# Performance work log

Measured on AMD Instinct MI355X. Metric: run time of the kernel, lower is better.

## Reference

```python
import jax, jax.numpy as jnp
import numpy as np

D_MODEL = 2048
N_HEADS = 16
HEAD_DIM = 128
WINDOW = 256
B, T = 2, 2048
SCALE = float(np.sqrt(HEAD_DIM))


def setup_inputs() -> dict:
    key = jax.random.key(0)
    ks = jax.random.split(key, 5)
    init = 0.02
    x = jax.random.normal(ks[0], (B, T, D_MODEL), dtype=jnp.float32)
    Wq = jax.random.normal(ks[1], (D_MODEL, D_MODEL), dtype=jnp.float32) * init
    Wk = jax.random.normal(ks[2], (D_MODEL, D_MODEL), dtype=jnp.float32) * init
    Wv = jax.random.normal(ks[3], (D_MODEL, D_MODEL), dtype=jnp.float32) * init
    Wo = jax.random.normal(ks[4], (D_MODEL, D_MODEL), dtype=jnp.float32) * init
    return {"x": x, "Wq": Wq, "Wk": Wk, "Wv": Wv, "Wo": Wo}


def _allowed_mask():
    # [H, T, T] bool: global (even) heads -> causal; local (odd) heads -> causal band of WINDOW
    idx = jnp.arange(T)
    causal = idx[None, :] <= idx[:, None]                      # [T, T]
    band = idx[None, :] >= (idx[:, None] - WINDOW + 1)         # [T, T]
    is_global = (jnp.arange(N_HEADS) % 2) == 0                 # [H]
    return causal[None] & (is_global[:, None, None] | band[None])


def reference(x, Wq, Wk, Wv, Wo):
    # projections (nn.Linear: y = x @ W.T), reshape to [B, H, T, D]
    def proj(W):
        return (x @ W.T).reshape(B, T, N_HEADS, HEAD_DIM).transpose(0, 2, 1, 3)

    q, k, v = proj(Wq), proj(Wk), proj(Wv)
    scores = jnp.einsum("bhtd,bhsd->bhts", q, k) / SCALE       # [B, H, T, T]
    allowed = _allowed_mask()                                  # [H, T, T]
    neg_inf = jnp.asarray(-jnp.inf, dtype=scores.dtype)
    scores = jnp.where(allowed[None], scores, neg_inf)
    attn = jax.nn.softmax(scores, axis=-1)
    out = jnp.einsum("bhts,bhsd->bhtd", attn, v)               # [B, H, T, D]
    concat = out.transpose(0, 2, 1, 3).reshape(B, T, N_HEADS * HEAD_DIM)
    return concat @ Wo.T
```

## Files before the change

kernel.cpp:

```cpp
#include <hip/hip_runtime.h>

typedef __attribute__((ext_vector_type(4))) float f32x4;
typedef __attribute__((ext_vector_type(8))) short bf16x8;
typedef __attribute__((ext_vector_type(4))) unsigned short u16x4;
typedef unsigned short u16;

#define MFMA16(a, b, c) __builtin_amdgcn_mfma_f32_16x16x32_bf16((a), (b), (c), 0, 0, 0)

#define T_SEQ 2048
#define DMODEL 2048
#define NHEADS 16
#define HDIM 128
#define WINDOW 256
#define MROWS 4096
#define SC 0.08838834764831845f

__device__ __forceinline__ u16 f2bf(float f) {
  union { float f; unsigned u; } v; v.f = f;
  return (u16)((v.u + 0x7FFFu + ((v.u >> 16) & 1u)) >> 16);
}
__device__ __forceinline__ float bf2f(u16 u) {
  union { unsigned u; float f; } v; v.u = ((unsigned)u) << 16;
  return v.f;
}
__device__ __forceinline__ void gl_lds16(const u16* g, u16* l) {
  __builtin_amdgcn_global_load_lds((const __attribute__((address_space(1))) void*)(g),
                                   (__attribute__((address_space(3))) void*)(l), 16, 0, 0);
}

#define BAR __builtin_amdgcn_s_barrier()
#define FEN asm volatile("" ::: "memory")
#define VMC3 asm volatile("s_waitcnt vmcnt(3)" ::: "memory")
#define VMC2 asm volatile("s_waitcnt vmcnt(2)" ::: "memory")
#define VMC0 asm volatile("s_waitcnt vmcnt(0)" ::: "memory")

__global__ __launch_bounds__(256) void convert_all(const float* __restrict__ x,
                                                   const float* __restrict__ wq,
                                                   const float* __restrict__ wk,
                                                   const float* __restrict__ wv,
                                                   const float* __restrict__ wo,
                                                   u16* __restrict__ dst) {
  const size_t NX = (size_t)MROWS * DMODEL;
  const size_t NW = (size_t)DMODEL * DMODEL;
  const size_t chunks = (NX + 4 * NW) / 8;
  for (size_t ci = (size_t)blockIdx.x * 256 + threadIdx.x; ci < chunks;
       ci += (size_t)gridDim.x * 256) {
    const size_t off = ci * 8;
    const float* src;
    size_t so;
    if (off < NX) { src = x; so = off; }
    else {
      size_t rem = off - NX;
      if (rem < NW) { src = wq; so = rem; }
      else if (rem < 2 * NW) { src = wk; so = rem - NW; }
      else if (rem < 3 * NW) { src = wv; so = rem - 2 * NW; }
      else { src = wo; so = rem - 3 * NW; }
    }
    f32x4 a = *(const f32x4*)&src[so];
    f32x4 b = *(const f32x4*)&src[so + 4];
    bf16x8 o;
#pragma unroll
    for (int j = 0; j < 4; ++j) { o[j] = (short)f2bf(a[j]); o[j + 4] = (short)f2bf(b[j]); }
    *(bf16x8*)&dst[off] = o;
  }
}

__global__ __launch_bounds__(512, 2) void gemm_qkv(const u16* __restrict__ A,
                                                   const u16* __restrict__ W,
                                                   u16* __restrict__ qb,
                                                   u16* __restrict__ kb,
                                                   u16* __restrict__ vb) {
  __shared__ u16 lds[57344];
  const int tid = threadIdx.x, w = tid >> 6, lane = tid & 63;
  const int wm = w >> 2, wn = w & 3;
  const int fr = lane & 15, g = lane >> 4, g4 = g * 4;

  const int xcd = blockIdx.x & 7, bi = blockIdx.x >> 3;
  const int mt = bi >> 2, nt = xcd * 4 + (bi & 3);
  const int m0 = mt * 256, n0 = nt * 192;

  const int xs0 = (g ^ (fr & 7)) * 8;
  const int xs1 = xs0 ^ 32;
  const int aRow = wm * 128 + fr;
  const int bRow = wn * 48 + fr;

  const int sr = tid >> 3;
  const int scc = ((tid & 7) ^ (sr & 7)) * 8;
  const u16* pA0  = A + (size_t)(m0 + sr) * DMODEL + scc;
  const u16* pA1  = A + (size_t)(m0 + 64 + sr) * DMODEL + scc;
  const u16* pB0  = W + (size_t)(n0 + sr) * DMODEL + scc;
  const u16* pB0b = W + (size_t)(n0 + 64 + sr) * DMODEL + scc;
  const u16* pB1  = W + (size_t)(n0 + 128 + sr) * DMODEL + scc;

#define SAH(h, t, c)                                                                   \
  { gl_lds16(pA0 + (size_t)(h) * 128 * DMODEL + (t) * 64,                              \
             &lds[(c) * 16384 + (h) * 8192 + w * 512]);                                \
    gl_lds16(pA1 + (size_t)(h) * 128 * DMODEL + (t) * 64,                              \
             &lds[(c) * 16384 + (h) * 8192 + 4096 + w * 512]); }
#define SBH0(t, c)                                                                     \
  { gl_lds16(pB0 + (size_t)(t) * 64, &lds[32768 + (c) * 12288 + w * 512]);             \
    gl_lds16(pB0b + (size_t)(t) * 64, &lds[32768 + (c) * 12288 + 4096 + w * 512]); }
#define SBH1(t, c)                                                                     \
  { gl_lds16(pB1 + (size_t)(t) * 64, &lds[32768 + (c) * 12288 + 8192 + w * 512]); }

#define RD_AL(c)                                                                       \
  { _Pragma("unroll") for (int m_ = 0; m_ < 4; ++m_) {                                 \
      af[m_][0] = *(const bf16x8*)&lds[(c) * 16384 + (aRow + m_ * 16) * 64 + xs0];     \
      af[m_][1] = *(const bf16x8*)&lds[(c) * 16384 + (aRow + m_ * 16) * 64 + xs1]; } }
#define RD_AH(c)                                                                       \
  { _Pragma("unroll") for (int m_ = 0; m_ < 4; ++m_) {                                 \
      af[m_][0] = *(const bf16x8*)&lds[(c) * 16384 + (aRow + 64 + m_ * 16) * 64 + xs0];\
      af[m_][1] = *(const bf16x8*)&lds[(c) * 16384 + (aRow + 64 + m_ * 16) * 64 + xs1]; } }
#define RD_B(c)                                                                        \
  { _Pragma("unroll") for (int n_ = 0; n_ < 3; ++n_) {                                 \
      bfr[n_][0] = *(const bf16x8*)&lds[32768 + (c) * 12288 + (bRow + n_ * 16) * 64 + xs0]; \
      bfr[n_][1] = *(const bf16x8*)&lds[32768 + (c) * 12288 + (bRow + n_ * 16) * 64 + xs1]; } }

#define MMQ(MB)                                                                        \
  { __builtin_amdgcn_s_setprio(1);                                                    \
    _Pragma("unroll") for (int kc_ = 0; kc_ < 2; ++kc_)                                \
      _Pragma("unroll") for (int m_ = 0; m_ < 4; ++m_)                                 \
        _Pragma("unroll") for (int n_ = 0; n_ < 3; ++n_)                               \
          acc[(MB) + m_][n_] = MFMA16(af[m_][kc_], bfr[n_][kc_], acc[(MB) + m_][n_]);  \
    __builtin_amdgcn_s_setprio(0); }

  bf16x8 af[4][2], bfr[3][2];
  f32x4 acc[8][3];
#pragma unroll
  for (int i = 0; i < 8; ++i)
#pragma unroll
    for (int j = 0; j < 3; ++j) acc[i][j] = (f32x4){0.f, 0.f, 0.f, 0.f};

  SAH(0, 0, 0); SAH(1, 0, 0);
  SBH0(0, 0); SBH1(0, 0);
  SBH0(1, 1); SBH1(1, 1);
  VMC3; BAR;

#pragma unroll 1
  for (int i = 0; i < 15; ++i) {
    const int t0 = 2 * i;
    RD_AL(0); RD_B(0); SAH(0, t0 + 1, 1); SAH(1, t0 + 1, 1);
    FEN; BAR; MMQ(0); FEN; BAR;
    RD_AH(0); SBH0(t0 + 2, 0); SBH1(t0 + 2, 0);
    VMC3; BAR; MMQ(4); FEN; BAR;
    RD_AL(1); RD_B(1); SAH(0, t0 + 2, 0); SAH(1, t0 + 2, 0);
    FEN; BAR; MMQ(0); FEN; BAR;
    RD_AH(1); SBH0(t0 + 3, 1); SBH1(t0 + 3, 1);
    VMC3; BAR; MMQ(4); FEN; BAR;
  }
  RD_AL(0); RD_B(0); SAH(0, 31, 1); SAH(1, 31, 1);
  FEN; BAR; MMQ(0); FEN; BAR;
  RD_AH(0);
  VMC0; BAR; MMQ(4); FEN; BAR;
  RD_AL(1); RD_B(1);
  FEN; BAR; MMQ(0); FEN; BAR;
  RD_AH(1);
  FEN; BAR; MMQ(4);

#pragma unroll
  for (int mi = 0; mi < 8; ++mi)
#pragma unroll
    for (int ni = 0; ni < 3; ++ni) {
      const int row0 = m0 + wm * 128 + mi * 16 + g4;
      const int cg = n0 + wn * 48 + ni * 16 + fr;
      const int bb = row0 >> 11, tl = row0 & 2047;
      if (cg < DMODEL) {
#pragma unroll
        for (int r = 0; r < 4; ++r)
          qb[(size_t)(row0 + r) * DMODEL + cg] = f2bf(acc[mi][ni][r] * SC);
      } else if (cg < 2 * DMODEL) {
        const int cc = cg - DMODEL;
        const int hh = cc >> 7, d = cc & 127;
        const size_t kbase = (size_t)(bb * NHEADS + hh) * T_SEQ * HDIM;
#pragma unroll
        for (int r = 0; r < 4; ++r)
          kb[kbase + (size_t)(tl + r) * HDIM + d] = f2bf(acc[mi][ni][r]);
      } else {
        const int cc = cg - 2 * DMODEL;
        const int hh = cc >> 7, d = cc & 127;
        u16x4 w4;
#pragma unroll
        for (int r = 0; r < 4; ++r) w4[r] = f2bf(acc[mi][ni][r]);
        *(u16x4*)&vb[(size_t)(bb * NHEADS + hh) * T_SEQ * HDIM + (size_t)(tl >> 6) * 8192 +
                     d * 64 + (tl & 63)] = w4;
      }
    }
#undef SAH
#undef SBH0
#undef SBH1
#undef RD_AL
#undef RD_AH
#undef RD_B
#undef MMQ
}

__global__ __launch_bounds__(512, 2) void gemm_out(const u16* __restrict__ A,
                                                   const u16* __restrict__ W0,
                                                   float* __restrict__ outf) {
  __shared__ u16 lds2[49152];
  const int tid = threadIdx.x, w = tid >> 6, lane = tid & 63;
  const int wm = w >> 2, wn = w & 3;
  const int fr = lane & 15, g = lane >> 4, g4 = g * 4;

  const int xcd = blockIdx.x & 7, bi = blockIdx.x >> 3;
  const int mt = bi >> 1, nt = xcd * 2 + (bi & 1);
  const int m0 = mt * 256, n0 = nt * 128;

  const int xs0 = (g ^ (fr & 7)) * 8;
  const int xs1 = xs0 ^ 32;
  const int aRow = wm * 128 + fr;
  const int bRow = wn * 32 + fr;

  const int sr = tid >> 3;
  const int scc = ((tid & 7) ^ (sr & 7)) * 8;
  const u16* pA0  = A + (size_t)(m0 + sr) * DMODEL + scc;
  const u16* pA1  = A + (size_t)(m0 + 64 + sr) * DMODEL + scc;
  const u16* pB0  = W0 + (size_t)(n0 + sr) * DMODEL + scc;
  const u16* pB0b = W0 + (size_t)(n0 + 64 + sr) * DMODEL + scc;

#define S2A(h, t, c)                                                                   \
  { gl_lds16(pA0 + (size_t)(h) * 128 * DMODEL + (t) * 64,                              \
             &lds2[(c) * 16384 + (h) * 8192 + w * 512]);                               \
    gl_lds16(pA1 + (size_t)(h) * 128 * DMODEL + (t) * 64,                              \
             &lds2[(c) * 16384 + (h) * 8192 + 4096 + w * 512]); }
#define S2B(t, c)                                                                      \
  { gl_lds16(pB0 + (size_t)(t) * 64, &lds2[32768 + (c) * 8192 + w * 512]);             \
    gl_lds16(pB0b + (size_t)(t) * 64, &lds2[32768 + (c) * 8192 + 4096 + w * 512]); }

#define R2AL(c)                                                                        \
  { _Pragma("unroll") for (int m_ = 0; m_ < 4; ++m_) {                                 \
      af[m_][0] = *(const bf16x8*)&lds2[(c) * 16384 + (aRow + m_ * 16) * 64 + xs0];    \
      af[m_][1] = *(const bf16x8*)&lds2[(c) * 16384 + (aRow + m_ * 16) * 64 + xs1]; } }
#define R2AH(c)                                                                        \
  { _Pragma("unroll") for (int m_ = 0; m_ < 4; ++m_) {                                 \
      af[m_][0] = *(const bf16x8*)&lds2[(c) * 16384 + (aRow + 64 + m_ * 16) * 64 + xs0]; \
      af[m_][1] = *(const bf16x8*)&lds2[(c) * 16384 + (aRow + 64 + m_ * 16) * 64 + xs1]; } }
#define R2B(c)                                                                         \
  { _Pragma("unroll") for (int n_ = 0; n_ < 2; ++n_) {                                 \
      bfr[n_][0] = *(const bf16x8*)&lds2[32768 + (c) * 8192 + (bRow + n_ * 16) * 64 + xs0]; \
      bfr[n_][1] = *(const bf16x8*)&lds2[32768 + (c) * 8192 + (bRow + n_ * 16) * 64 + xs1]; } }

#define M2(MB)                                                                         \
  { __builtin_amdgcn_s_setprio(1);                                                    \
    _Pragma("unroll") for (int kc_ = 0; kc_ < 2; ++kc_)                                \
      _Pragma("unroll") for (int m_ = 0; m_ < 4; ++m_)                                 \
        _Pragma("unroll") for (int n_ = 0; n_ < 2; ++n_)                               \
          acc[(MB) + m_][n_] = MFMA16(af[m_][kc_], bfr[n_][kc_], acc[(MB) + m_][n_]);  \
    __builtin_amdgcn_s_setprio(0); }

  bf16x8 af[4][2], bfr[2][2];
  f32x4 acc[8][2];
#pragma unroll
  for (int i = 0; i < 8; ++i)
#pragma unroll
    for (int j = 0; j < 2; ++j) acc[i][j] = (f32x4){0.f, 0.f, 0.f, 0.f};

  S2A(0, 0, 0); S2A(1, 0, 0);
  S2B(0, 0);
  S2B(1, 1);
  VMC2; BAR;

#pragma unroll 1
  for (int i = 0; i < 15; ++i) {
    const int t0 = 2 * i;
    R2AL(0); R2B(0); S2A(0, t0 + 1, 1); S2A(1, t0 + 1, 1);
    FEN; BAR; M2(0); FEN; BAR;
    R2AH(0); S2B(t0 + 2, 0);
    VMC2; BAR; M2(4); FEN; BAR;
    R2AL(1); R2B(1); S2A(0, t0 + 2, 0); S2A(1, t0 + 2, 0);
    FEN; BAR; M2(0); FEN; BAR;
    R2AH(1); S2B(t0 + 3, 1);
    VMC2; BAR; M2(4); FEN; BAR;
  }
  R2AL(0); R2B(0); S2A(0, 31, 1); S2A(1, 31, 1);
  FEN; BAR; M2(0); FEN; BAR;
  R2AH(0);
  VMC0; BAR; M2(4); FEN; BAR;
  R2AL(1); R2B(1);
  FEN; BAR; M2(0); FEN; BAR;
  R2AH(1);
  FEN; BAR; M2(4);

#pragma unroll
  for (int mi = 0; mi < 8; ++mi)
#pragma unroll
    for (int ni = 0; ni < 2; ++ni) {
      const int row0 = m0 + wm * 128 + mi * 16 + g4;
      const int c = n0 + wn * 32 + ni * 16 + fr;
#pragma unroll
      for (int r = 0; r < 4; ++r)
        outf[(size_t)(row0 + r) * DMODEL + c] = acc[mi][ni][r];
    }
#undef S2A
#undef S2B
#undef R2AL
#undef R2AH
#undef R2B
#undef M2
}

#define QB 128
#define KVB 64

__global__ __launch_bounds__(512, 4) void attn_kernel(const u16* __restrict__ qb,
                                                      const u16* __restrict__ kb,
                                                      const u16* __restrict__ vb,
                                                      u16* __restrict__ op,
                                                      u16* __restrict__ pO,
                                                      float* __restrict__ pm,
                                                      float* __restrict__ pl) {
  __shared__ u16 lds[40960];

  const int bx = blockIdx.x, h = blockIdx.y, b = blockIdx.z;
  const bool isglobal = (h & 1) == 0;
  int qt, klo, khi, part = 0;
  bool partial = false;
  if (isglobal) {
    if (bx < 16) {
      qt = 15 - (bx >> 1);
      part = bx & 1;
      partial = true;
      if (part == 0) { klo = 0; khi = 15; } else { klo = 16; khi = 2 * qt + 1; }
    } else {
      qt = 23 - bx;
      klo = 0; khi = 2 * qt + 1;
    }
  } else {
    if (bx >= 16) return;
    qt = 15 - bx;
    const int lo_ = qt * QB - (WINDOW - 1);
    klo = lo_ > 0 ? (lo_ >> 6) : 0;
    khi = 2 * qt + 1;
  }

  const int tid = threadIdx.x, wave = tid >> 6, lane = tid & 63;
  const int fr = lane & 15, g = lane >> 4, g4 = g * 4;
  const int xk = fr & 7;
  const int q0 = qt * QB;
  const int bh = b * NHEADS + h;
  const size_t basek = (size_t)bh * T_SEQ * HDIM;
  const size_t baseo = (size_t)b * T_SEQ * DMODEL + (size_t)h * HDIM;

  bf16x8 qf[4];
  {
    const int qrow = q0 + wave * 16 + fr;
#pragma unroll
    for (int ds = 0; ds < 4; ++ds)
      qf[ds] = *(const bf16x8*)&qb[(size_t)b * T_SEQ * DMODEL + (size_t)qrow * DMODEL +
                                   (size_t)h * HDIM + ds * 32 + g * 8];
  }

  float mrun = -1e30f, lrun = 0.f;
  f32x4 o[8];
#pragma unroll
  for (int dt = 0; dt < 8; ++dt) o[dt] = (f32x4){0.f, 0.f, 0.f, 0.f};

  const int j0 = wave * 2, j1 = wave * 2 + 1;
  const int gi0 = j0 * 64 + lane, gi1 = j1 * 64 + lane;
  const int kr0 = gi0 >> 4, kc0 = (gi0 & 15) ^ (kr0 & 7);
  const int kr1 = gi1 >> 4, kc1 = (gi1 & 15) ^ (kr1 & 7);
  const u16* pK0 = kb + basek + (size_t)kr0 * HDIM + kc0 * 8;
  const u16* pK1 = kb + basek + (size_t)kr1 * HDIM + kc1 * 8;
  const int d0 = gi0 >> 3, vs0 = (gi0 & 7) ^ (d0 & 7);
  const int d1 = gi1 >> 3, vs1 = (gi1 & 7) ^ (d1 & 7);
  const u16* pV0 = vb + basek + (size_t)d0 * 64 + vs0 * 8;
  const u16* pV1 = vb + basek + (size_t)d1 * 64 + vs1 * 8;

#define STAGE(KT, c)                                                                   \
  { gl_lds16(pK0 + (size_t)(KT) * 8192, &lds[(c) * 8192 + j0 * 512]);                  \
    gl_lds16(pK1 + (size_t)(KT) * 8192, &lds[(c) * 8192 + j1 * 512]);                  \
    gl_lds16(pV0 + (size_t)(KT) * 8192, &lds[16384 + (c) * 8192 + j0 * 512]);          \
    gl_lds16(pV1 + (size_t)(KT) * 8192, &lds[16384 + (c) * 8192 + j1 * 512]); }

  u16* Pw = &lds[32768 + wave * 1024];
  const int qg = q0 + wave * 16 + fr;

  STAGE(klo, klo & 1);
  VMC0; BAR;

  for (int kt = klo; kt <= khi; ++kt) {
    const int c = kt & 1;
    const bool more = kt < khi;
    if (more) STAGE(kt + 1, c ^ 1);
    const u16* Kc = &lds[c * 8192];
    const u16* Vc = &lds[16384 + c * 8192];

    f32x4 s[4];
    __builtin_amdgcn_s_setprio(1);
#pragma unroll
    for (int kk = 0; kk < 4; ++kk) {
      f32x4 a = (f32x4){0.f, 0.f, 0.f, 0.f};
#pragma unroll
      for (int ds = 0; ds < 4; ++ds) {
        const int r = kk * 16 + fr;
        bf16x8 kf = *(const bf16x8*)&Kc[r * 128 + (((ds * 4 + g) ^ xk) << 3)];
        a = MFMA16(kf, qf[ds], a);
      }
      s[kk] = a;
    }
    __builtin_amdgcn_s_setprio(0);

    float sv[16];
    float pmax = -1e30f;
#pragma unroll
    for (int kk = 0; kk < 4; ++kk)
#pragma unroll
      for (int reg = 0; reg < 4; ++reg) {
        const int cg = kt * KVB + kk * 16 + g4 + reg;
        const bool allowed = (cg <= qg) && (isglobal || cg >= qg - (WINDOW - 1));
        const float v = allowed ? s[kk][reg] : -1e30f;
        sv[kk * 4 + reg] = v;
        pmax = fmaxf(pmax, v);
      }
    pmax = fmaxf(pmax, __shfl_xor(pmax, 16, 64));
    pmax = fmaxf(pmax, __shfl_xor(pmax, 32, 64));
    const bool resc = !__all(pmax - mrun <= 8.0f);
    float fac = 1.f;
    if (resc) {
      const float nm = fmaxf(mrun, pmax);
      fac = __expf(mrun - nm);
      mrun = nm;
    }
    float rs = 0.f;
    u16 pb[16];
#pragma unroll
    for (int i = 0; i < 16; ++i) {
      const float p = (sv[i] > -5e29f) ? __expf(sv[i] - mrun) : 0.f;
      rs += p;
      pb[i] = f2bf(p);
    }
    rs += __shfl_xor(rs, 16, 64);
    rs += __shfl_xor(rs, 32, 64);
    lrun = lrun * fac + rs;

#pragma unroll
    for (int kk = 0; kk < 4; ++kk) {
      u16x4 wv;
      wv[0] = pb[kk * 4]; wv[1] = pb[kk * 4 + 1]; wv[2] = pb[kk * 4 + 2]; wv[3] = pb[kk * 4 + 3];
      *(u16x4*)&Pw[fr * 64 + (((2 * kk + (g >> 1)) ^ xk) << 3) + (g & 1) * 4] = wv;
    }

    if (resc) {
      float ff[4];
#pragma unroll
      for (int r = 0; r < 4; ++r) ff[r] = __shfl(fac, g4 + r, 64);
#pragma unroll
      for (int dt = 0; dt < 8; ++dt)
#pragma unroll
        for (int r = 0; r < 4; ++r) o[dt][r] *= ff[r];
    }

    bf16x8 pf0 = *(const bf16x8*)&Pw[fr * 64 + ((g ^ xk) << 3)];
    bf16x8 pf1 = *(const bf16x8*)&Pw[fr * 64 + (((4 + g) ^ xk) << 3)];
    __builtin_amdgcn_s_setprio(1);
#pragma unroll
    for (int dt = 0; dt < 8; ++dt) {
      const int d = dt * 16 + fr;
      bf16x8 vf0 = *(const bf16x8*)&Vc[d * 64 + ((g ^ xk) << 3)];
      bf16x8 vf1 = *(const bf16x8*)&Vc[d * 64 + (((4 + g) ^ xk) << 3)];
      o[dt] = MFMA16(pf0, vf0, o[dt]);
      o[dt] = MFMA16(pf1, vf1, o[dt]);
    }
    __builtin_amdgcn_s_setprio(0);

    FEN;
    VMC0;
    BAR;
  }

  if (!partial) {
    const float inv = 1.0f / lrun;
    float iv[4];
#pragma unroll
    for (int r = 0; r < 4; ++r) iv[r] = __shfl(inv, g4 + r, 64);
#pragma unroll
    for (int r = 0; r < 4; ++r) {
      const int qrow = q0 + wave * 16 + g4 + r;
#pragma unroll
      for (int dt = 0; dt < 8; ++dt)
        op[baseo + (size_t)qrow * DMODEL + dt * 16 + fr] = f2bf(o[dt][r] * iv[r]);
    }
  } else {
    const int sidx = (((b * 8 + (h >> 1)) * 8 + (qt - 8)) << 1) + part;
    const size_t sb = (size_t)sidx * QB;
#pragma unroll
    for (int r = 0; r < 4; ++r) {
      const size_t row = sb + wave * 16 + g4 + r;
#pragma unroll
      for (int dt = 0; dt < 8; ++dt)
        pO[row * HDIM + dt * 16 + fr] = f2bf(o[dt][r]);
    }
    if (lane < 16) {
      pm[sb + wave * 16 + lane] = mrun;
      pl[sb + wave * 16 + lane] = lrun;
    }
  }
#undef STAGE
}

__global__ __launch_bounds__(256) void merge_kernel(const u16* __restrict__ pO,
                                                    const float* __restrict__ pm,
                                                    const float* __restrict__ pl,
                                                    u16* __restrict__ op) {
  const int x = blockIdx.x;
  const int qt8 = x & 7, eh = (x >> 3) & 7, b = x >> 6;
  const int h = eh * 2, qt = 8 + qt8;
  const int s0 = x * 2, s1 = s0 + 1;

  for (int i = 0; i < 8; ++i) {
    const int vidx = threadIdx.x + i * 256;
    const int row = vidx >> 4, d8 = (vidx & 15) * 8;
    const float m0 = pm[s0 * QB + row], m1 = pm[s1 * QB + row];
    const float l0 = pl[s0 * QB + row], l1 = pl[s1 * QB + row];
    const float m = fmaxf(m0, m1);
    const float w0 = __expf(m0 - m), w1 = __expf(m1 - m);
    const float inv = 1.0f / (l0 * w0 + l1 * w1);
    bf16x8 a = *(const bf16x8*)&pO[((size_t)s0 * QB + row) * HDIM + d8];
    bf16x8 c = *(const bf16x8*)&pO[((size_t)s1 * QB + row) * HDIM + d8];
    bf16x8 r;
#pragma unroll
    for (int j = 0; j < 8; ++j)
      r[j] = (short)f2bf((bf2f((u16)a[j]) * w0 + bf2f((u16)c[j]) * w1) * inv);
    *(bf16x8*)&op[((size_t)(b * T_SEQ + qt * QB + row)) * DMODEL + h * HDIM + d8] = r;
  }
}

extern "C" void kernel_launch(void* const* d_in, const int* in_sizes, int n_in,
                              void* d_out, int out_size, void* d_ws, size_t ws_size,
                              hipStream_t stream) {
  (void)in_sizes; (void)n_in; (void)out_size; (void)ws_size;
  const float* x  = (const float*)d_in[0];
  const float* Wq = (const float*)d_in[1];
  const float* Wk = (const float*)d_in[2];
  const float* Wv = (const float*)d_in[3];
  const float* Wo = (const float*)d_in[4];

  const size_t NX = (size_t)MROWS * DMODEL;
  const size_t NW = (size_t)DMODEL * DMODEL;
  u16* ws  = (u16*)d_ws;
  u16* xb  = ws;
  u16* wqb = ws + NX;
  u16* wkb = wqb + NW;
  u16* wvb = wkb + NW;
  u16* wob = wvb + NW;
  u16* qbb = wob + NW;
  u16* kbb = qbb + NX;
  u16* vbb = kbb + NX;

  u16*   pO = wqb;
  float* pm = (float*)(wqb + (size_t)256 * QB * HDIM);
  float* pl = pm + 256 * QB;

  convert_all<<<2048, 256, 0, stream>>>(x, Wq, Wk, Wv, Wo, ws);

  gemm_qkv<<<512, 512, 0, stream>>>(xb, wqb, qbb, kbb, vbb);

  attn_kernel<<<dim3(24, NHEADS, 2), 512, 0, stream>>>(qbb, kbb, vbb, xb, pO, pm, pl);

  merge_kernel<<<128, 256, 0, stream>>>(pO, pm, pl, xb);

  gemm_out<<<256, 512, 0, stream>>>(xb, wob, (float*)d_out);
}
```

Baseline: 246.7 us.

## Process two 16-row query tiles per wave in attention with 4 waves per block

The attention kernel now runs 4 waves (256 threads) per block, and each wave handles 32 query rows as two 16-row sub-tiles. Each K fragment read from LDS feeds two QK MFMAs and each V fragment feeds two PV MFMAs, halving LDS reads per MFMA. Each wave also issues twice as many global-to-LDS staging loads. Register pressure roughly doubles for accumulators and Q fragments, and there are fewer waves per block to hide latency.

```diff
diff --git a/kernel.cpp b/kernel.cpp
--- a/kernel.cpp
+++ b/kernel.cpp
@@ -302,7 +302,7 @@
 #define QB 128
 #define KVB 64
 
-__global__ __launch_bounds__(512, 4) void attn_kernel(const u16* __restrict__ qb,
+__global__ __launch_bounds__(256, 2) void attn_kernel(const u16* __restrict__ qb,
                                                       const u16* __restrict__ kb,
                                                       const u16* __restrict__ vb,
                                                       u16* __restrict__ op,
@@ -341,39 +341,47 @@
   const size_t basek = (size_t)bh * T_SEQ * HDIM;
   const size_t baseo = (size_t)b * T_SEQ * DMODEL + (size_t)h * HDIM;
 
-  bf16x8 qf[4];
+  bf16x8 qf0[4], qf1[4];
   {
-    const int qrow = q0 + wave * 16 + fr;
-#pragma unroll
-    for (int ds = 0; ds < 4; ++ds)
-      qf[ds] = *(const bf16x8*)&qb[(size_t)b * T_SEQ * DMODEL + (size_t)qrow * DMODEL +
-                                   (size_t)h * HDIM + ds * 32 + g * 8];
-  }
-
-  float mrun = -1e30f, lrun = 0.f;
-  f32x4 o[8];
-#pragma unroll
-  for (int dt = 0; dt < 8; ++dt) o[dt] = (f32x4){0.f, 0.f, 0.f, 0.f};
-
-  const int j0 = wave * 2, j1 = wave * 2 + 1;
-  const int gi0 = j0 * 64 + lane, gi1 = j1 * 64 + lane;
-  const int kr0 = gi0 >> 4, kc0 = (gi0 & 15) ^ (kr0 & 7);
-  const int kr1 = gi1 >> 4, kc1 = (gi1 & 15) ^ (kr1 & 7);
-  const u16* pK0 = kb + basek + (size_t)kr0 * HDIM + kc0 * 8;
-  const u16* pK1 = kb + basek + (size_t)kr1 * HDIM + kc1 * 8;
-  const int d0 = gi0 >> 3, vs0 = (gi0 & 7) ^ (d0 & 7);
-  const int d1 = gi1 >> 3, vs1 = (gi1 & 7) ^ (d1 & 7);
-  const u16* pV0 = vb + basek + (size_t)d0 * 64 + vs0 * 8;
-  const u16* pV1 = vb + basek + (size_t)d1 * 64 + vs1 * 8;
+    const int qr0 = q0 + wave * 32 + fr;
+#pragma unroll
+    for (int ds = 0; ds < 4; ++ds) {
+      qf0[ds] = *(const bf16x8*)&qb[(size_t)b * T_SEQ * DMODEL + (size_t)qr0 * DMODEL +
+                                    (size_t)h * HDIM + ds * 32 + g * 8];
+      qf1[ds] = *(const bf16x8*)&qb[(size_t)b * T_SEQ * DMODEL + (size_t)(qr0 + 16) * DMODEL +
+                                    (size_t)h * HDIM + ds * 32 + g * 8];
+    }
+  }
+
+  float mr0 = -1e30f, lr0 = 0.f, mr1 = -1e30f, lr1 = 0.f;
+  f32x4 o0[8], o1[8];
+#pragma unroll
+  for (int dt = 0; dt < 8; ++dt) {
+    o0[dt] = (f32x4){0.f, 0.f, 0.f, 0.f};
+    o1[dt] = (f32x4){0.f, 0.f, 0.f, 0.f};
+  }
+
+  const u16* pK[4];
+  const u16* pV[4];
+#pragma unroll
+  for (int j = 0; j < 4; ++j) {
+    const int gi = (wave * 4 + j) * 64 + lane;
+    const int kr = gi >> 4, kc = (gi & 15) ^ (kr & 7);
+    pK[j] = kb + basek + (size_t)kr * HDIM + kc * 8;
+    const int d = gi >> 3, vs = (gi & 7) ^ (d & 7);
+    pV[j] = vb + basek + (size_t)d * 64 + vs * 8;
+  }
 
 #define STAGE(KT, c)                                                                   \
-  { gl_lds16(pK0 + (size_t)(KT) * 8192, &lds[(c) * 8192 + j0 * 512]);                  \
-    gl_lds16(pK1 + (size_t)(KT) * 8192, &lds[(c) * 8192 + j1 * 512]);                  \
-    gl_lds16(pV0 + (size_t)(KT) * 8192, &lds[16384 + (c) * 8192 + j0 * 512]);          \
-    gl_lds16(pV1 + (size_t)(KT) * 8192, &lds[16384 + (c) * 8192 + j1 * 512]); }
-
-  u16* Pw = &lds[32768 + wave * 1024];
-  const int qg = q0 + wave * 16 + fr;
+  { _Pragma("unroll") for (int j = 0; j < 4; ++j) {                                    \
+      gl_lds16(pK[j] + (size_t)(KT) * 8192, &lds[(c) * 8192 + (wave * 4 + j) * 512]);  \
+      gl_lds16(pV[j] + (size_t)(KT) * 8192,                                            \
+               &lds[16384 + (c) * 8192 + (wave * 4 + j) * 512]); } }
+
+  u16* Pw0 = &lds[32768 + (wave * 2 + 0) * 1024];
+  u16* Pw1 = &lds[32768 + (wave * 2 + 1) * 1024];
+  const int qg0 = q0 + wave * 32 + fr;
+  const int qg1 = qg0 + 16;
 
   STAGE(klo, klo & 1);
   VMC0; BAR;
@@ -385,81 +393,87 @@
     const u16* Kc = &lds[c * 8192];
     const u16* Vc = &lds[16384 + c * 8192];
 
-    f32x4 s[4];
+    f32x4 s0[4], s1[4];
     __builtin_amdgcn_s_setprio(1);
 #pragma unroll
     for (int kk = 0; kk < 4; ++kk) {
-      f32x4 a = (f32x4){0.f, 0.f, 0.f, 0.f};
+      f32x4 a0 = (f32x4){0.f, 0.f, 0.f, 0.f};
+      f32x4 a1 = (f32x4){0.f, 0.f, 0.f, 0.f};
 #pragma unroll
       for (int ds = 0; ds < 4; ++ds) {
         const int r = kk * 16 + fr;
         bf16x8 kf = *(const bf16x8*)&Kc[r * 128 + (((ds * 4 + g) ^ xk) << 3)];
-        a = MFMA16(kf, qf[ds], a);
+        a0 = MFMA16(kf, qf0[ds], a0);
+        a1 = MFMA16(kf, qf1[ds], a1);
       }
-      s[kk] = a;
+      s0[kk] = a0;
+      s1[kk] = a1;
     }
     __builtin_amdgcn_s_setprio(0);
 
-    float sv[16];
-    float pmax = -1e30f;
-#pragma unroll
-    for (int kk = 0; kk < 4; ++kk)
-#pragma unroll
-      for (int reg = 0; reg < 4; ++reg) {
-        const int cg = kt * KVB + kk * 16 + g4 + reg;
-        const bool allowed = (cg <= qg) && (isglobal || cg >= qg - (WINDOW - 1));
-        const float v = allowed ? s[kk][reg] : -1e30f;
-        sv[kk * 4 + reg] = v;
-        pmax = fmaxf(pmax, v);
-      }
-    pmax = fmaxf(pmax, __shfl_xor(pmax, 16, 64));
-    pmax = fmaxf(pmax, __shfl_xor(pmax, 32, 64));
-    const bool resc = !__all(pmax - mrun <= 8.0f);
-    float fac = 1.f;
-    if (resc) {
-      const float nm = fmaxf(mrun, pmax);
-      fac = __expf(mrun - nm);
-      mrun = nm;
-    }
-    float rs = 0.f;
-    u16 pb[16];
-#pragma unroll
-    for (int i = 0; i < 16; ++i) {
-      const float p = (sv[i] > -5e29f) ? __expf(sv[i] - mrun) : 0.f;
-      rs += p;
-      pb[i] = f2bf(p);
-    }
-    rs += __shfl_xor(rs, 16, 64);
-    rs += __shfl_xor(rs, 32, 64);
-    lrun = lrun * fac + rs;
-
-#pragma unroll
-    for (int kk = 0; kk < 4; ++kk) {
-      u16x4 wv;
-      wv[0] = pb[kk * 4]; wv[1] = pb[kk * 4 + 1]; wv[2] = pb[kk * 4 + 2]; wv[3] = pb[kk * 4 + 3];
-      *(u16x4*)&Pw[fr * 64 + (((2 * kk + (g >> 1)) ^ xk) << 3) + (g & 1) * 4] = wv;
-    }
-
-    if (resc) {
-      float ff[4];
-#pragma unroll
-      for (int r = 0; r < 4; ++r) ff[r] = __shfl(fac, g4 + r, 64);
-#pragma unroll
-      for (int dt = 0; dt < 8; ++dt)
-#pragma unroll
-        for (int r = 0; r < 4; ++r) o[dt][r] *= ff[r];
-    }
-
-    bf16x8 pf0 = *(const bf16x8*)&Pw[fr * 64 + ((g ^ xk) << 3)];
-    bf16x8 pf1 = *(const bf16x8*)&Pw[fr * 64 + (((4 + g) ^ xk) << 3)];
+#define SOFTMAX(SARR, MR, LR, PW, OA, QG)                                              \
+    {                                                                                  \
+      float sv[16];                                                                    \
+      float pmax = -1e30f;                                                             \
+      _Pragma("unroll") for (int kk = 0; kk < 4; ++kk)                                 \
+        _Pragma("unroll") for (int reg = 0; reg < 4; ++reg) {                          \
+          const int cg = kt * KVB + kk * 16 + g4 + reg;                                \
+          const bool allowed = (cg <= (QG)) && (isglobal || cg >= (QG) - (WINDOW - 1));\
+          const float v = allowed ? SARR[kk][reg] : -1e30f;                            \
+          sv[kk * 4 + reg] = v;                                                        \
+          pmax = fmaxf(pmax, v);                                                       \
+        }                                                                              \
+      pmax = fmaxf(pmax, __shfl_xor(pmax, 16, 64));                                    \
+      pmax = fmaxf(pmax, __shfl_xor(pmax, 32, 64));                                    \
+      const bool resc = !__all(pmax - MR <= 8.0f);                                     \
+      float fac = 1.f;                                                                 \
+      if (resc) {                                                                      \
+        const float nm = fmaxf(MR, pmax);                                              \
+        fac = __expf(MR - nm);                                                         \
+        MR = nm;                                                                       \
+      }                                                                                \
+      float rs = 0.f;                                                                  \
+      u16 pb[16];                                                                      \
+      _Pragma("unroll") for (int i = 0; i < 16; ++i) {                                 \
+        const float p = (sv[i] > -5e29f) ? __expf(sv[i] - MR) : 0.f;                   \
+        rs += p;                                                                       \
+        pb[i] = f2bf(p);                                                               \
+      }                                                                                \
+      rs += __shfl_xor(rs, 16, 64);                                                    \
+      rs += __shfl_xor(rs, 32, 64);                                                    \
+      LR = LR * fac + rs;                                                              \
+      _Pragma("unroll") for (int kk = 0; kk < 4; ++kk) {                               \
+        u16x4 wv;                                                                      \
+        wv[0] = pb[kk * 4]; wv[1] = pb[kk * 4 + 1];                                    \
+        wv[2] = pb[kk * 4 + 2]; wv[3] = pb[kk * 4 + 3];                                \
+        *(u16x4*)&PW[fr * 64 + (((2 * kk + (g >> 1)) ^ xk) << 3) + (g & 1) * 4] = wv;  \
+      }                                                                                \
+      if (resc) {                                                                      \
+        float ff[4];                                                                   \
+        _Pragma("unroll") for (int r = 0; r < 4; ++r) ff[r] = __shfl(fac, g4 + r, 64); \
+        _Pragma("unroll") for (int dt = 0; dt < 8; ++dt)                               \
+          _Pragma("unroll") for (int r = 0; r < 4; ++r) OA[dt][r] *= ff[r];            \
+      }                                                                                \
+    }
+
+    SOFTMAX(s0, mr0, lr0, Pw0, o0, qg0);
+    SOFTMAX(s1, mr1, lr1, Pw1, o1, qg1);
+#undef SOFTMAX
+
+    bf16x8 pf00 = *(const bf16x8*)&Pw0[fr * 64 + ((g ^ xk) << 3)];
+    bf16x8 pf01 = *(const bf16x8*)&Pw0[fr * 64 + (((4 + g) ^ xk) << 3)];
+    bf16x8 pf10 = *(const bf16x8*)&Pw1[fr * 64 + ((g ^ xk) << 3)];
+    bf16x8 pf11 = *(const bf16x8*)&Pw1[fr * 64 + (((4 + g) ^ xk) << 3)];
     __builtin_amdgcn_s_setprio(1);
 #pragma unroll
     for (int dt = 0; dt < 8; ++dt) {
       const int d = dt * 16 + fr;
       bf16x8 vf0 = *(const bf16x8*)&Vc[d * 64 + ((g ^ xk) << 3)];
       bf16x8 vf1 = *(const bf16x8*)&Vc[d * 64 + (((4 + g) ^ xk) << 3)];
-      o[dt] = MFMA16(pf0, vf0, o[dt]);
-      o[dt] = MFMA16(pf1, vf1, o[dt]);
+      o0[dt] = MFMA16(pf00, vf0, o0[dt]);
+      o0[dt] = MFMA16(pf01, vf1, o0[dt]);
+      o1[dt] = MFMA16(pf10, vf0, o1[dt]);
+      o1[dt] = MFMA16(pf11, vf1, o1[dt]);
     }
     __builtin_amdgcn_s_setprio(0);
 
@@ -469,30 +483,39 @@
   }
 
   if (!partial) {
-    const float inv = 1.0f / lrun;
-    float iv[4];
-#pragma unroll
-    for (int r = 0; r < 4; ++r) iv[r] = __shfl(inv, g4 + r, 64);
+    const float i0 = 1.0f / lr0, i1 = 1.0f / lr1;
+    float iv0[4], iv1[4];
 #pragma unroll
     for (int r = 0; r < 4; ++r) {
-      const int qrow = q0 + wave * 16 + g4 + r;
-#pragma unroll
-      for (int dt = 0; dt < 8; ++dt)
-        op[baseo + (size_t)qrow * DMODEL + dt * 16 + fr] = f2bf(o[dt][r] * iv[r]);
+      iv0[r] = __shfl(i0, g4 + r, 64);
+      iv1[r] = __shfl(i1, g4 + r, 64);
+    }
+#pragma unroll
+    for (int r = 0; r < 4; ++r) {
+      const int qr0 = q0 + wave * 32 + g4 + r;
+#pragma unroll
+      for (int dt = 0; dt < 8; ++dt) {
+        op[baseo + (size_t)qr0 * DMODEL + dt * 16 + fr] = f2bf(o0[dt][r] * iv0[r]);
+        op[baseo + (size_t)(qr0 + 16) * DMODEL + dt * 16 + fr] = f2bf(o1[dt][r] * iv1[r]);
+      }
     }
   } else {
     const int sidx = (((b * 8 + (h >> 1)) * 8 + (qt - 8)) << 1) + part;
     const size_t sb = (size_t)sidx * QB;
 #pragma unroll
     for (int r = 0; r < 4; ++r) {
-      const size_t row = sb + wave * 16 + g4 + r;
-#pragma unroll
-      for (int dt = 0; dt < 8; ++dt)
-        pO[row * HDIM + dt * 16 + fr] = f2bf(o[dt][r]);
+      const size_t row0 = sb + wave * 32 + g4 + r;
+#pragma unroll
+      for (int dt = 0; dt < 8; ++dt) {
+        pO[row0 * HDIM + dt * 16 + fr] = f2bf(o0[dt][r]);
+        pO[(row0 + 16) * HDIM + dt * 16 + fr] = f2bf(o1[dt][r]);
+      }
     }
     if (lane < 16) {
-      pm[sb + wave * 16 + lane] = mrun;
-      pl[sb + wave * 16 + lane] = lrun;
+      pm[sb + wave * 32 + lane] = mr0;
+      pm[sb + wave * 32 + 16 + lane] = mr1;
+      pl[sb + wave * 32 + lane] = lr0;
+      pl[sb + wave * 32 + 16 + lane] = lr1;
     }
   }
 #undef STAGE
@@ -555,7 +578,7 @@
 
   gemm_qkv<<<512, 512, 0, stream>>>(xb, wqb, qbb, kbb, vbb);
 
-  attn_kernel<<<dim3(24, NHEADS, 2), 512, 0, stream>>>(qbb, kbb, vbb, xb, pO, pm, pl);
+  attn_kernel<<<dim3(24, NHEADS, 2), 256, 0, stream>>>(qbb, kbb, vbb, xb, pO, pm, pl);
 
   merge_kernel<<<128, 256, 0, stream>>>(pO, pm, pl, xb);
 
```

Result: slower. 258.1 us (+4.6%).
